# Optimization experiments

Hardware: AMD Instinct MI355X
Metric: run time of the kernel (lower is better)

The kernel has to match this reference:

```python
import jax, jax.numpy as jnp
import numpy as np

NUM_HEADS = 16
D_MODEL = 1024
DEPTH = D_MODEL // NUM_HEADS


def rope_sincos(seq_len, depth):
    # standard RoPE: inv_freq over even dims, sin/cos tiled to full depth
    inv_freq = 1.0 / (10000.0 ** (jnp.arange(0, depth, 2, dtype=jnp.float32) / depth))
    ang = jnp.arange(seq_len, dtype=jnp.float32)[:, None] * inv_freq[None, :]  # [S, depth/2]
    sin = jnp.concatenate([jnp.sin(ang), jnp.sin(ang)], axis=-1)  # [S, depth]
    cos = jnp.concatenate([jnp.cos(ang), jnp.cos(ang)], axis=-1)
    return sin, cos


def apply_rope(x, sin, cos):
    # x: [B,H,S,depth]; rotate-half formulation
    half = x.shape[-1] // 2
    x1, x2 = x[..., :half], x[..., half:]
    rot = jnp.concatenate([-x2, x1], axis=-1)
    return x * cos + rot * sin


def setup_inputs() -> dict:
    key = jax.random.key(0)
    ks = jax.random.split(key, 5)
    s = 1.0 / np.sqrt(D_MODEL)
    return {
        "x": jax.random.normal(ks[0], (2, 2048, D_MODEL), dtype=jnp.float32),
        "wq": jax.random.normal(ks[1], (D_MODEL, D_MODEL), dtype=jnp.float32) * s,
        "bq": jnp.zeros((D_MODEL,), jnp.float32),
        "wk": jax.random.normal(ks[2], (D_MODEL, D_MODEL), dtype=jnp.float32) * s,
        "bk": jnp.zeros((D_MODEL,), jnp.float32),
        "wv": jax.random.normal(ks[3], (D_MODEL, D_MODEL), dtype=jnp.float32) * s,
        "bv": jnp.zeros((D_MODEL,), jnp.float32),
        "wo": jax.random.normal(ks[4], (D_MODEL, D_MODEL), dtype=jnp.float32) * s,
        "bo": jnp.zeros((D_MODEL,), jnp.float32),
    }


def reference(x, wq, bq, wk, bk, wv, bv, wo, bo):
    B, S, _ = x.shape

    def split_heads(t):  # [B,S,D] -> [B,H,S,depth]
        return t.reshape(B, S, NUM_HEADS, DEPTH).transpose(0, 2, 1, 3)

    Q = split_heads(x @ wq + bq)
    K = split_heads(x @ wk + bk)
    V = split_heads(x @ wv + bv)

    sin, cos = rope_sincos(S, DEPTH)  # [S, depth], broadcasts over B,H
    Q = apply_rope(Q, sin, cos)
    K = apply_rope(K, sin, cos)

    scores = jnp.einsum("bhqd,bhkd->bhqk", Q, K) / jnp.sqrt(jnp.float32(DEPTH))
    weights = jax.nn.softmax(scores, axis=-1)
    out = jnp.einsum("bhqk,bhkd->bhqd", weights, V)
    out = out.transpose(0, 2, 1, 3).reshape(B, S, D_MODEL)
    return out @ wo + bo
```

## Files before the change

kernel.cpp:

```cpp
#include <hip/hip_runtime.h>

#define DM 1024
#define SEQ 2048
#define NH 16
#define DH 64
#define BATCH 2

typedef _Float16 half_t;
typedef _Float16 half8 __attribute__((ext_vector_type(8)));
typedef _Float16 half4 __attribute__((ext_vector_type(4)));
typedef float f32x4 __attribute__((ext_vector_type(4)));

__device__ __forceinline__ f32x4 mfma16(half8 a, half8 b, f32x4 c) {
  return __builtin_amdgcn_mfma_f32_16x16x32_f16(a, b, c, 0, 0, 0);
}

__device__ __forceinline__ void gl2lds16(const half_t* g, half_t* l) {
  __builtin_amdgcn_global_load_lds((const __attribute__((address_space(1))) void*)g,
                                   (__attribute__((address_space(3))) void*)l, 16, 0, 0);
}


__global__ void cvt_x_kernel(const float* __restrict__ x, half_t* __restrict__ xh) {
  int i = (blockIdx.x * 256 + threadIdx.x) * 4;
  float4 v = *(const float4*)(x + i);
  half4 h = { (half_t)v.x, (half_t)v.y, (half_t)v.z, (half_t)v.w };
  *(half4*)(xh + i) = h;
}

__global__ void wtrans_kernel(const float* __restrict__ w0, const float* __restrict__ w1,
                              const float* __restrict__ w2, const float* __restrict__ w3,
                              half_t* __restrict__ o0, half_t* __restrict__ o1,
                              half_t* __restrict__ o2, half_t* __restrict__ o3) {
  __shared__ float tile[32][33];
  const float* w = (blockIdx.z == 0) ? w0 : (blockIdx.z == 1) ? w1 : (blockIdx.z == 2) ? w2 : w3;
  half_t* o = (blockIdx.z == 0) ? o0 : (blockIdx.z == 1) ? o1 : (blockIdx.z == 2) ? o2 : o3;
  int tx = threadIdx.x, ty0 = threadIdx.y;
  int bx = blockIdx.x * 32, by = blockIdx.y * 32;
#pragma unroll
  for (int i = 0; i < 4; i++) {
    int ty = ty0 + i * 8;
    tile[ty][tx] = w[(size_t)(by + ty) * DM + bx + tx];
  }
  __syncthreads();
#pragma unroll
  for (int i = 0; i < 4; i++) {
    int ty = ty0 + i * 8;
    o[(size_t)(bx + ty) * DM + by + tx] = (half_t)tile[tx][ty];
  }
}

__global__ void ropetab_kernel(float* __restrict__ st, float* __restrict__ ct) {
  int idx = blockIdx.x * 256 + threadIdx.x;
  int s = idx >> 5, i = idx & 31;
  float freq = exp2f(-(float)i * (13.287712379549449f / 32.0f));
  float ang = (float)s * freq;
  st[idx] = sinf(ang);
  ct[idx] = cosf(ang);
}

__global__ __launch_bounds__(256)
void vtrans_kernel(const half_t* __restrict__ Vh, half_t* __restrict__ Vt) {
  __shared__ half_t t[64 * 72];
  const int tid = threadIdx.x;
  const int bh = blockIdx.y;
  const int s0 = blockIdx.x * 64;
  const half_t* src = Vh + (size_t)bh * SEQ * DH + (size_t)s0 * DH;
  half_t* dst = Vt + (size_t)bh * DH * SEQ;
#pragma unroll
  for (int i = 0; i < 2; i++) {
    int s = tid + i * 256;
    int row = s >> 3, blk = s & 7;
    *(half8*)&t[row * 72 + blk * 8] = *(const half8*)&src[(size_t)row * DH + blk * 8];
  }
  __syncthreads();
  const int d = tid >> 2;
#pragma unroll
  for (int i = 0; i < 2; i++) {
    int sb = (tid & 3) * 8 + i * 32;
    half8 v;
#pragma unroll
    for (int j = 0; j < 8; j++) v[j] = t[(sb + j) * 72 + d];
    *(half8*)&dst[(size_t)d * SEQ + s0 + sb] = v;
  }
}


__global__ __launch_bounds__(256)
void qkv_kernel(const half_t* __restrict__ xh,
                const half_t* __restrict__ wtq, const half_t* __restrict__ wtk,
                const half_t* __restrict__ wtv,
                const float* __restrict__ bq, const float* __restrict__ bk,
                const float* __restrict__ bv,
                const float* __restrict__ st, const float* __restrict__ ctab,
                half_t* __restrict__ Qh, half_t* __restrict__ Kh, half_t* __restrict__ Vh) {
  const int tid = threadIdx.x;
  const int wid = tid >> 6, lane = tid & 63;
  const int l16 = lane & 15, quad = lane >> 4;
  const int g = blockIdx.z;
  const int m0 = blockIdx.y * 128, n0 = blockIdx.x * 128;
  const half_t* wt = (g == 0) ? wtq : (g == 1) ? wtk : wtv;
  const float* bias = (g == 0) ? bq : (g == 1) ? bk : bv;
  __shared__ __align__(16) half_t As[128 * 64];
  __shared__ __align__(16) half_t Bs[128 * 64];
  f32x4 acc[4][4] = {};
  const int wrow = (wid >> 1) * 64, wcol = (wid & 1) * 64;

  const int r0 = tid >> 3,         b0 = (tid & 7) ^ (r0 & 7);
  const int r1 = (tid + 256) >> 3, b1 = (tid & 7) ^ (r1 & 7);
  const int r2 = (tid + 512) >> 3, b2 = (tid & 7) ^ (r2 & 7);
  const int r3 = (tid + 768) >> 3, b3 = (tid & 7) ^ (r3 & 7);
  const int pb0 = (quad ^ (l16 & 7)) * 8;
  const int pb1 = ((4 + quad) ^ (l16 & 7)) * 8;

  for (int k0 = 0; k0 < DM; k0 += 64) {
    __syncthreads();
    gl2lds16(&xh[(size_t)(m0 + r0) * DM + k0 + b0 * 8], &As[tid * 8]);
    gl2lds16(&xh[(size_t)(m0 + r1) * DM + k0 + b1 * 8], &As[(tid + 256) * 8]);
    gl2lds16(&xh[(size_t)(m0 + r2) * DM + k0 + b2 * 8], &As[(tid + 512) * 8]);
    gl2lds16(&xh[(size_t)(m0 + r3) * DM + k0 + b3 * 8], &As[(tid + 768) * 8]);
    gl2lds16(&wt[(size_t)(n0 + r0) * DM + k0 + b0 * 8], &Bs[tid * 8]);
    gl2lds16(&wt[(size_t)(n0 + r1) * DM + k0 + b1 * 8], &Bs[(tid + 256) * 8]);
    gl2lds16(&wt[(size_t)(n0 + r2) * DM + k0 + b2 * 8], &Bs[(tid + 512) * 8]);
    gl2lds16(&wt[(size_t)(n0 + r3) * DM + k0 + b3 * 8], &Bs[(tid + 768) * 8]);
    __syncthreads();
    half8 a[2][4], b[2][4];
#pragma unroll
    for (int rt = 0; rt < 4; rt++) {
      a[0][rt] = *(const half8*)&As[(wrow + rt * 16 + l16) * 64 + pb0];
      a[1][rt] = *(const half8*)&As[(wrow + rt * 16 + l16) * 64 + pb1];
    }
#pragma unroll
    for (int ct = 0; ct < 4; ct++) {
      b[0][ct] = *(const half8*)&Bs[(wcol + ct * 16 + l16) * 64 + pb0];
      b[1][ct] = *(const half8*)&Bs[(wcol + ct * 16 + l16) * 64 + pb1];
    }
#pragma unroll
    for (int kk = 0; kk < 2; kk++)
#pragma unroll
      for (int rt = 0; rt < 4; rt++)
#pragma unroll
        for (int ct = 0; ct < 4; ct++)
          acc[rt][ct] = mfma16(a[kk][rt], b[kk][ct], acc[rt][ct]);
  }

  const int h = (n0 + wcol) >> 6;
  const float qscale = 0.125f * 1.44269504089f;
  half_t* dst = (g == 0) ? Qh : (g == 1) ? Kh : Vh;
  float bv4[4];
#pragma unroll
  for (int ct = 0; ct < 4; ct++) bv4[ct] = bias[n0 + wcol + ct * 16 + l16];
#pragma unroll
  for (int rt = 0; rt < 4; rt++) {
#pragma unroll
    for (int r = 0; r < 4; r++) {
      int m = m0 + wrow + rt * 16 + quad * 4 + r;
      int bb = m >> 11, s = m & 2047;
      float v0 = acc[rt][0][r] + bv4[0];
      float v1 = acc[rt][1][r] + bv4[1];
      float v2 = acc[rt][2][r] + bv4[2];
      float v3 = acc[rt][3][r] + bv4[3];
      float o0 = v0, o1 = v1, o2 = v2, o3 = v3;
      if (g != 2) {
        float sn0 = st[s * 32 + l16], cs0 = ctab[s * 32 + l16];
        float sn1 = st[s * 32 + 16 + l16], cs1 = ctab[s * 32 + 16 + l16];
        o0 = v0 * cs0 - v2 * sn0;
        o1 = v1 * cs1 - v3 * sn1;
        o2 = v2 * cs0 + v0 * sn0;
        o3 = v3 * cs1 + v1 * sn1;
        if (g == 0) { o0 *= qscale; o1 *= qscale; o2 *= qscale; o3 *= qscale; }
      }
      size_t base = ((size_t)(bb * NH + h) * SEQ + s) * DH;
      dst[base + l16]      = (half_t)o0;
      dst[base + 16 + l16] = (half_t)o1;
      dst[base + 32 + l16] = (half_t)o2;
      dst[base + 48 + l16] = (half_t)o3;
    }
  }
}


__global__ __launch_bounds__(256)
void attn_kernel(const half_t* __restrict__ Qh, const half_t* __restrict__ Kh,
                 const half_t* __restrict__ Vt, half_t* __restrict__ AO) {
  const int tid = threadIdx.x;
  const int wid = tid >> 6, lane = tid & 63;
  const int l16 = lane & 15, quad = lane >> 4;
  const int bh = blockIdx.x;
  const int bb = bh >> 4, h = bh & 15;
  const int q0 = blockIdx.y * 128 + wid * 32;
  const half_t* Q = Qh + (size_t)bh * SEQ * DH;
  const half_t* K = Kh + (size_t)bh * SEQ * DH;
  const half_t* V = Vt + (size_t)bh * DH * SEQ;
  __shared__ __align__(16) half_t Ks[64 * 64];
  __shared__ __align__(16) half_t Vs[64 * 64];
  __shared__ __align__(16) half_t pbuf[4][32 * 72];
  half_t* myp = pbuf[wid];

  const int r0 = tid >> 3,         c0 = (tid & 7) ^ (r0 & 7);
  const int r1 = (tid + 256) >> 3, c1 = (tid & 7) ^ (r1 & 7);
  const int sw0 = ((quad ^ (l16 & 7)) * 8);
  const int sw1 = (((quad + 4) ^ (l16 & 7)) * 8);

  half8 aqA0 = *(const half8*)&Q[(size_t)(q0 + l16) * DH + quad * 8];
  half8 aqA1 = *(const half8*)&Q[(size_t)(q0 + l16) * DH + 32 + quad * 8];
  half8 aqB0 = *(const half8*)&Q[(size_t)(q0 + 16 + l16) * DH + quad * 8];
  half8 aqB1 = *(const half8*)&Q[(size_t)(q0 + 16 + l16) * DH + 32 + quad * 8];
  f32x4 oA[4] = {}, oB[4] = {};
  float lrowA[4] = {0.f, 0.f, 0.f, 0.f}, lrowB[4] = {0.f, 0.f, 0.f, 0.f};
  const f32x4 cinit = {-12.f, -12.f, -12.f, -12.f};

  for (int kb0 = 0; kb0 < SEQ; kb0 += 64) {
    __syncthreads();
    gl2lds16(&K[(size_t)(kb0 + r0) * DH + c0 * 8], &Ks[tid * 8]);
    gl2lds16(&K[(size_t)(kb0 + r1) * DH + c1 * 8], &Ks[(tid + 256) * 8]);
    gl2lds16(&V[(size_t)r0 * SEQ + kb0 + c0 * 8], &Vs[tid * 8]);
    gl2lds16(&V[(size_t)r1 * SEQ + kb0 + c1 * 8], &Vs[(tid + 256) * 8]);
    __syncthreads();

    f32x4 sfA[4], sfB[4];
#pragma unroll
    for (int kt = 0; kt < 4; kt++) {
      const half_t* krow = &Ks[(kt * 16 + l16) * 64];
      half8 b0 = *(const half8*)&krow[sw0];
      half8 b1 = *(const half8*)&krow[sw1];
      f32x4 zA = cinit, zB = cinit;
      zA = mfma16(aqA0, b0, zA);
      zA = mfma16(aqA1, b1, zA);
      zB = mfma16(aqB0, b0, zB);
      zB = mfma16(aqB1, b1, zB);
      sfA[kt] = zA; sfB[kt] = zB;
    }
#pragma unroll
    for (int kt = 0; kt < 4; kt++)
#pragma unroll
      for (int r = 0; r < 4; r++) {
        float pA = __builtin_amdgcn_exp2f(sfA[kt][r]);
        float pB = __builtin_amdgcn_exp2f(sfB[kt][r]);
        lrowA[r] += pA;
        lrowB[r] += pB;
        myp[(quad * 4 + r) * 72 + kt * 16 + l16] = (half_t)pA;
        myp[(16 + quad * 4 + r) * 72 + kt * 16 + l16] = (half_t)pB;
      }
    half8 apA0 = *(const half8*)&myp[l16 * 72 + quad * 8];
    half8 apA1 = *(const half8*)&myp[l16 * 72 + 32 + quad * 8];
    half8 apB0 = *(const half8*)&myp[(16 + l16) * 72 + quad * 8];
    half8 apB1 = *(const half8*)&myp[(16 + l16) * 72 + 32 + quad * 8];
#pragma unroll
    for (int dt = 0; dt < 4; dt++) {
      const half_t* vrow = &Vs[(dt * 16 + l16) * 64];
      half8 bv0 = *(const half8*)&vrow[sw0];
      half8 bv1 = *(const half8*)&vrow[sw1];
      oA[dt] = mfma16(apA0, bv0, oA[dt]);
      oA[dt] = mfma16(apA1, bv1, oA[dt]);
      oB[dt] = mfma16(apB0, bv0, oB[dt]);
      oB[dt] = mfma16(apB1, bv1, oB[dt]);
    }
  }
#pragma unroll
  for (int d = 1; d <= 8; d <<= 1)
#pragma unroll
    for (int r = 0; r < 4; r++) {
      lrowA[r] += __shfl_xor(lrowA[r], d);
      lrowB[r] += __shfl_xor(lrowB[r], d);
    }
#pragma unroll
  for (int r = 0; r < 4; r++) { lrowA[r] = 1.f / lrowA[r]; lrowB[r] = 1.f / lrowB[r]; }
#pragma unroll
  for (int dt = 0; dt < 4; dt++)
#pragma unroll
    for (int r = 0; r < 4; r++) {
      int srowA = q0 + quad * 4 + r;
      int srowB = q0 + 16 + quad * 4 + r;
      AO[((size_t)bb * SEQ + srowA) * DM + h * DH + dt * 16 + l16] = (half_t)(oA[dt][r] * lrowA[r]);
      AO[((size_t)bb * SEQ + srowB) * DM + h * DH + dt * 16 + l16] = (half_t)(oB[dt][r] * lrowB[r]);
    }
}


__global__ __launch_bounds__(256)
void out_kernel(const half_t* __restrict__ AO, const half_t* __restrict__ wto,
                const float* __restrict__ bo, float* __restrict__ out) {
  const int tid = threadIdx.x;
  const int wid = tid >> 6, lane = tid & 63;
  const int l16 = lane & 15, quad = lane >> 4;
  const int m0 = blockIdx.y * 128, n0 = blockIdx.x * 64;
  __shared__ __align__(16) half_t As[128 * 64];
  __shared__ __align__(16) half_t Bs[64 * 64];
  f32x4 acc[4][2] = {};
  const int wrow = (wid >> 1) * 64, wcol = (wid & 1) * 32;

  const int r0 = tid >> 3,         b0 = (tid & 7) ^ (r0 & 7);
  const int r1 = (tid + 256) >> 3, b1 = (tid & 7) ^ (r1 & 7);
  const int r2 = (tid + 512) >> 3, b2 = (tid & 7) ^ (r2 & 7);
  const int r3 = (tid + 768) >> 3, b3 = (tid & 7) ^ (r3 & 7);
  const int pb0 = (quad ^ (l16 & 7)) * 8;
  const int pb1 = ((4 + quad) ^ (l16 & 7)) * 8;

  for (int k0 = 0; k0 < DM; k0 += 64) {
    __syncthreads();
    gl2lds16(&AO[(size_t)(m0 + r0) * DM + k0 + b0 * 8], &As[tid * 8]);
    gl2lds16(&AO[(size_t)(m0 + r1) * DM + k0 + b1 * 8], &As[(tid + 256) * 8]);
    gl2lds16(&AO[(size_t)(m0 + r2) * DM + k0 + b2 * 8], &As[(tid + 512) * 8]);
    gl2lds16(&AO[(size_t)(m0 + r3) * DM + k0 + b3 * 8], &As[(tid + 768) * 8]);
    gl2lds16(&wto[(size_t)(n0 + r0) * DM + k0 + b0 * 8], &Bs[tid * 8]);
    gl2lds16(&wto[(size_t)(n0 + r1) * DM + k0 + b1 * 8], &Bs[(tid + 256) * 8]);
    __syncthreads();
    half8 a[2][4], b[2][2];
#pragma unroll
    for (int rt = 0; rt < 4; rt++) {
      a[0][rt] = *(const half8*)&As[(wrow + rt * 16 + l16) * 64 + pb0];
      a[1][rt] = *(const half8*)&As[(wrow + rt * 16 + l16) * 64 + pb1];
    }
#pragma unroll
    for (int ct = 0; ct < 2; ct++) {
      b[0][ct] = *(const half8*)&Bs[(wcol + ct * 16 + l16) * 64 + pb0];
      b[1][ct] = *(const half8*)&Bs[(wcol + ct * 16 + l16) * 64 + pb1];
    }
#pragma unroll
    for (int kk = 0; kk < 2; kk++)
#pragma unroll
      for (int rt = 0; rt < 4; rt++)
#pragma unroll
        for (int ct = 0; ct < 2; ct++)
          acc[rt][ct] = mfma16(a[kk][rt], b[kk][ct], acc[rt][ct]);
  }
  float bv2[2];
#pragma unroll
  for (int ct = 0; ct < 2; ct++) bv2[ct] = bo[n0 + wcol + ct * 16 + l16];
#pragma unroll
  for (int rt = 0; rt < 4; rt++)
#pragma unroll
    for (int r = 0; r < 4; r++) {
      int m = m0 + wrow + rt * 16 + quad * 4 + r;
#pragma unroll
      for (int ct = 0; ct < 2; ct++)
        out[(size_t)m * DM + n0 + wcol + ct * 16 + l16] = acc[rt][ct][r] + bv2[ct];
    }
}


extern "C" void kernel_launch(void* const* d_in, const int* in_sizes, int n_in,
                              void* d_out, int out_size, void* d_ws, size_t ws_size,
                              hipStream_t stream) {
  (void)in_sizes; (void)n_in; (void)out_size; (void)ws_size;
  const float* x  = (const float*)d_in[0];
  const float* wq = (const float*)d_in[1];
  const float* bq = (const float*)d_in[2];
  const float* wk = (const float*)d_in[3];
  const float* bk = (const float*)d_in[4];
  const float* wv = (const float*)d_in[5];
  const float* bv = (const float*)d_in[6];
  const float* wo = (const float*)d_in[7];
  const float* bo = (const float*)d_in[8];
  char* ws = (char*)d_ws;
  const size_t MB = 1u << 20;
  half_t* xh  = (half_t*)(ws + 0);
  half_t* AO  = (half_t*)(ws + 0);
  half_t* wtq = (half_t*)(ws + 8 * MB);
  half_t* wtk = (half_t*)(ws + 10 * MB);
  half_t* wtv = (half_t*)(ws + 12 * MB);
  half_t* wto = (half_t*)(ws + 14 * MB);
  float*  st  = (float*)(ws + 16 * MB);
  float*  ctb = (float*)(ws + 16 * MB + 256 * 1024);
  half_t* Qh  = (half_t*)(ws + 17 * MB);
  half_t* Kh  = (half_t*)(ws + 25 * MB);
  half_t* Vh  = (half_t*)(ws + 33 * MB);
  half_t* Vt  = (half_t*)(ws + 41 * MB);
  float* out = (float*)d_out;

  cvt_x_kernel<<<4096, 256, 0, stream>>>(x, xh);
  wtrans_kernel<<<dim3(32, 32, 4), dim3(32, 8), 0, stream>>>(wq, wk, wv, wo, wtq, wtk, wtv, wto);
  ropetab_kernel<<<256, 256, 0, stream>>>(st, ctb);
  qkv_kernel<<<dim3(8, 32, 3), 256, 0, stream>>>(xh, wtq, wtk, wtv, bq, bk, bv, st, ctb, Qh, Kh, Vh);
  vtrans_kernel<<<dim3(32, 32), 256, 0, stream>>>(Vh, Vt);
  attn_kernel<<<dim3(32, 16), 256, 0, stream>>>(Qh, Kh, Vt, AO);
  out_kernel<<<dim3(16, 32), 256, 0, stream>>>(AO, wto, bo, out);
}
```

Before: 218.6 us.

## Double-buffer LDS tiles in QKV, attention and output kernels

```diff
diff --git a/kernel.cpp b/kernel.cpp
--- a/kernel.cpp
+++ b/kernel.cpp
@@ -101,47 +101,42 @@
   const int m0 = blockIdx.y * 128, n0 = blockIdx.x * 128;
   const half_t* wt = (g == 0) ? wtq : (g == 1) ? wtk : wtv;
   const float* bias = (g == 0) ? bq : (g == 1) ? bk : bv;
-  __shared__ __align__(16) half_t As[128 * 64];
-  __shared__ __align__(16) half_t Bs[128 * 64];
+  __shared__ __align__(16) half_t As[2][128 * 32];
+  __shared__ __align__(16) half_t Bs[2][128 * 32];
   f32x4 acc[4][4] = {};
   const int wrow = (wid >> 1) * 64, wcol = (wid & 1) * 64;
 
-  const int r0 = tid >> 3,         b0 = (tid & 7) ^ (r0 & 7);
-  const int r1 = (tid + 256) >> 3, b1 = (tid & 7) ^ (r1 & 7);
-  const int r2 = (tid + 512) >> 3, b2 = (tid & 7) ^ (r2 & 7);
-  const int r3 = (tid + 768) >> 3, b3 = (tid & 7) ^ (r3 & 7);
-  const int pb0 = (quad ^ (l16 & 7)) * 8;
-  const int pb1 = ((4 + quad) ^ (l16 & 7)) * 8;
-
-  for (int k0 = 0; k0 < DM; k0 += 64) {
+  const int ar0 = tid >> 2,          ab0 = (tid & 3) ^ ((ar0 >> 1) & 3);
+  const int ar1 = (tid + 256) >> 2,  ab1 = (tid & 3) ^ ((ar1 >> 1) & 3);
+  const int swz = (l16 >> 1) & 3;
+
+  gl2lds16(&xh[(size_t)(m0 + ar0) * DM + ab0 * 8], &As[0][tid * 8]);
+  gl2lds16(&xh[(size_t)(m0 + ar1) * DM + ab1 * 8], &As[0][(tid + 256) * 8]);
+  gl2lds16(&wt[(size_t)(n0 + ar0) * DM + ab0 * 8], &Bs[0][tid * 8]);
+  gl2lds16(&wt[(size_t)(n0 + ar1) * DM + ab1 * 8], &Bs[0][(tid + 256) * 8]);
+
+  int cur = 0;
+  for (int k0 = 0; k0 < DM; k0 += 32, cur ^= 1) {
     __syncthreads();
-    gl2lds16(&xh[(size_t)(m0 + r0) * DM + k0 + b0 * 8], &As[tid * 8]);
-    gl2lds16(&xh[(size_t)(m0 + r1) * DM + k0 + b1 * 8], &As[(tid + 256) * 8]);
-    gl2lds16(&xh[(size_t)(m0 + r2) * DM + k0 + b2 * 8], &As[(tid + 512) * 8]);
-    gl2lds16(&xh[(size_t)(m0 + r3) * DM + k0 + b3 * 8], &As[(tid + 768) * 8]);
-    gl2lds16(&wt[(size_t)(n0 + r0) * DM + k0 + b0 * 8], &Bs[tid * 8]);
-    gl2lds16(&wt[(size_t)(n0 + r1) * DM + k0 + b1 * 8], &Bs[(tid + 256) * 8]);
-    gl2lds16(&wt[(size_t)(n0 + r2) * DM + k0 + b2 * 8], &Bs[(tid + 512) * 8]);
-    gl2lds16(&wt[(size_t)(n0 + r3) * DM + k0 + b3 * 8], &Bs[(tid + 768) * 8]);
-    __syncthreads();
-    half8 a[2][4], b[2][4];
-#pragma unroll
-    for (int rt = 0; rt < 4; rt++) {
-      a[0][rt] = *(const half8*)&As[(wrow + rt * 16 + l16) * 64 + pb0];
-      a[1][rt] = *(const half8*)&As[(wrow + rt * 16 + l16) * 64 + pb1];
-    }
-#pragma unroll
-    for (int ct = 0; ct < 4; ct++) {
-      b[0][ct] = *(const half8*)&Bs[(wcol + ct * 16 + l16) * 64 + pb0];
-      b[1][ct] = *(const half8*)&Bs[(wcol + ct * 16 + l16) * 64 + pb1];
-    }
-#pragma unroll
-    for (int kk = 0; kk < 2; kk++)
-#pragma unroll
-      for (int rt = 0; rt < 4; rt++)
-#pragma unroll
-        for (int ct = 0; ct < 4; ct++)
-          acc[rt][ct] = mfma16(a[kk][rt], b[kk][ct], acc[rt][ct]);
+    int kn = k0 + 32;
+    if (kn < DM) {
+      gl2lds16(&xh[(size_t)(m0 + ar0) * DM + kn + ab0 * 8], &As[cur ^ 1][tid * 8]);
+      gl2lds16(&xh[(size_t)(m0 + ar1) * DM + kn + ab1 * 8], &As[cur ^ 1][(tid + 256) * 8]);
+      gl2lds16(&wt[(size_t)(n0 + ar0) * DM + kn + ab0 * 8], &Bs[cur ^ 1][tid * 8]);
+      gl2lds16(&wt[(size_t)(n0 + ar1) * DM + kn + ab1 * 8], &Bs[cur ^ 1][(tid + 256) * 8]);
+    }
+    half8 a[4], b[4];
+#pragma unroll
+    for (int rt = 0; rt < 4; rt++)
+      a[rt] = *(const half8*)&As[cur][((wrow + rt * 16 + l16) * 4 + (quad ^ swz)) * 8];
+#pragma unroll
+    for (int ct = 0; ct < 4; ct++)
+      b[ct] = *(const half8*)&Bs[cur][((wcol + ct * 16 + l16) * 4 + (quad ^ swz)) * 8];
+#pragma unroll
+    for (int rt = 0; rt < 4; rt++)
+#pragma unroll
+      for (int ct = 0; ct < 4; ct++)
+        acc[rt][ct] = mfma16(a[rt], b[ct], acc[rt][ct]);
   }
 
   const int h = (n0 + wcol) >> 6;
@@ -192,8 +187,8 @@
   const half_t* Q = Qh + (size_t)bh * SEQ * DH;
   const half_t* K = Kh + (size_t)bh * SEQ * DH;
   const half_t* V = Vt + (size_t)bh * DH * SEQ;
-  __shared__ __align__(16) half_t Ks[64 * 64];
-  __shared__ __align__(16) half_t Vs[64 * 64];
+  __shared__ __align__(16) half_t Ks[2][64 * 64];
+  __shared__ __align__(16) half_t Vs[2][64 * 64];
   __shared__ __align__(16) half_t pbuf[4][32 * 72];
   half_t* myp = pbuf[wid];
 
@@ -210,18 +205,26 @@
   float lrowA[4] = {0.f, 0.f, 0.f, 0.f}, lrowB[4] = {0.f, 0.f, 0.f, 0.f};
   const f32x4 cinit = {-12.f, -12.f, -12.f, -12.f};
 
-  for (int kb0 = 0; kb0 < SEQ; kb0 += 64) {
+  gl2lds16(&K[(size_t)r0 * DH + c0 * 8], &Ks[0][tid * 8]);
+  gl2lds16(&K[(size_t)r1 * DH + c1 * 8], &Ks[0][(tid + 256) * 8]);
+  gl2lds16(&V[(size_t)r0 * SEQ + c0 * 8], &Vs[0][tid * 8]);
+  gl2lds16(&V[(size_t)r1 * SEQ + c1 * 8], &Vs[0][(tid + 256) * 8]);
+
+  int cur = 0;
+  for (int kb0 = 0; kb0 < SEQ; kb0 += 64, cur ^= 1) {
     __syncthreads();
-    gl2lds16(&K[(size_t)(kb0 + r0) * DH + c0 * 8], &Ks[tid * 8]);
-    gl2lds16(&K[(size_t)(kb0 + r1) * DH + c1 * 8], &Ks[(tid + 256) * 8]);
-    gl2lds16(&V[(size_t)r0 * SEQ + kb0 + c0 * 8], &Vs[tid * 8]);
-    gl2lds16(&V[(size_t)r1 * SEQ + kb0 + c1 * 8], &Vs[(tid + 256) * 8]);
-    __syncthreads();
+    int kn = kb0 + 64;
+    if (kn < SEQ) {
+      gl2lds16(&K[(size_t)(kn + r0) * DH + c0 * 8], &Ks[cur ^ 1][tid * 8]);
+      gl2lds16(&K[(size_t)(kn + r1) * DH + c1 * 8], &Ks[cur ^ 1][(tid + 256) * 8]);
+      gl2lds16(&V[(size_t)r0 * SEQ + kn + c0 * 8], &Vs[cur ^ 1][tid * 8]);
+      gl2lds16(&V[(size_t)r1 * SEQ + kn + c1 * 8], &Vs[cur ^ 1][(tid + 256) * 8]);
+    }
 
     f32x4 sfA[4], sfB[4];
 #pragma unroll
     for (int kt = 0; kt < 4; kt++) {
-      const half_t* krow = &Ks[(kt * 16 + l16) * 64];
+      const half_t* krow = &Ks[cur][(kt * 16 + l16) * 64];
       half8 b0 = *(const half8*)&krow[sw0];
       half8 b1 = *(const half8*)&krow[sw1];
       f32x4 zA = cinit, zB = cinit;
@@ -248,7 +251,7 @@
     half8 apB1 = *(const half8*)&myp[(16 + l16) * 72 + 32 + quad * 8];
 #pragma unroll
     for (int dt = 0; dt < 4; dt++) {
-      const half_t* vrow = &Vs[(dt * 16 + l16) * 64];
+      const half_t* vrow = &Vs[cur][(dt * 16 + l16) * 64];
       half8 bv0 = *(const half8*)&vrow[sw0];
       half8 bv1 = *(const half8*)&vrow[sw1];
       oA[dt] = mfma16(apA0, bv0, oA[dt]);
@@ -285,45 +288,40 @@
   const int wid = tid >> 6, lane = tid & 63;
   const int l16 = lane & 15, quad = lane >> 4;
   const int m0 = blockIdx.y * 128, n0 = blockIdx.x * 64;
-  __shared__ __align__(16) half_t As[128 * 64];
-  __shared__ __align__(16) half_t Bs[64 * 64];
+  __shared__ __align__(16) half_t As[2][128 * 32];
+  __shared__ __align__(16) half_t Bs[2][64 * 32];
   f32x4 acc[4][2] = {};
   const int wrow = (wid >> 1) * 64, wcol = (wid & 1) * 32;
 
-  const int r0 = tid >> 3,         b0 = (tid & 7) ^ (r0 & 7);
-  const int r1 = (tid + 256) >> 3, b1 = (tid & 7) ^ (r1 & 7);
-  const int r2 = (tid + 512) >> 3, b2 = (tid & 7) ^ (r2 & 7);
-  const int r3 = (tid + 768) >> 3, b3 = (tid & 7) ^ (r3 & 7);
-  const int pb0 = (quad ^ (l16 & 7)) * 8;
-  const int pb1 = ((4 + quad) ^ (l16 & 7)) * 8;
-
-  for (int k0 = 0; k0 < DM; k0 += 64) {
+  const int ar0 = tid >> 2,         ab0 = (tid & 3) ^ ((ar0 >> 1) & 3);
+  const int ar1 = (tid + 256) >> 2, ab1 = (tid & 3) ^ ((ar1 >> 1) & 3);
+  const int swz = (l16 >> 1) & 3;
+
+  gl2lds16(&AO[(size_t)(m0 + ar0) * DM + ab0 * 8], &As[0][tid * 8]);
+  gl2lds16(&AO[(size_t)(m0 + ar1) * DM + ab1 * 8], &As[0][(tid + 256) * 8]);
+  gl2lds16(&wto[(size_t)(n0 + ar0) * DM + ab0 * 8], &Bs[0][tid * 8]);
+
+  int cur = 0;
+  for (int k0 = 0; k0 < DM; k0 += 32, cur ^= 1) {
     __syncthreads();
-    gl2lds16(&AO[(size_t)(m0 + r0) * DM + k0 + b0 * 8], &As[tid * 8]);
-    gl2lds16(&AO[(size_t)(m0 + r1) * DM + k0 + b1 * 8], &As[(tid + 256) * 8]);
-    gl2lds16(&AO[(size_t)(m0 + r2) * DM + k0 + b2 * 8], &As[(tid + 512) * 8]);
-    gl2lds16(&AO[(size_t)(m0 + r3) * DM + k0 + b3 * 8], &As[(tid + 768) * 8]);
-    gl2lds16(&wto[(size_t)(n0 + r0) * DM + k0 + b0 * 8], &Bs[tid * 8]);
-    gl2lds16(&wto[(size_t)(n0 + r1) * DM + k0 + b1 * 8], &Bs[(tid + 256) * 8]);
-    __syncthreads();
-    half8 a[2][4], b[2][2];
-#pragma unroll
-    for (int rt = 0; rt < 4; rt++) {
-      a[0][rt] = *(const half8*)&As[(wrow + rt * 16 + l16) * 64 + pb0];
-      a[1][rt] = *(const half8*)&As[(wrow + rt * 16 + l16) * 64 + pb1];
-    }
-#pragma unroll
-    for (int ct = 0; ct < 2; ct++) {
-      b[0][ct] = *(const half8*)&Bs[(wcol + ct * 16 + l16) * 64 + pb0];
-      b[1][ct] = *(const half8*)&Bs[(wcol + ct * 16 + l16) * 64 + pb1];
-    }
-#pragma unroll
-    for (int kk = 0; kk < 2; kk++)
-#pragma unroll
-      for (int rt = 0; rt < 4; rt++)
-#pragma unroll
-        for (int ct = 0; ct < 2; ct++)
-          acc[rt][ct] = mfma16(a[kk][rt], b[kk][ct], acc[rt][ct]);
+    int kn = k0 + 32;
+    if (kn < DM) {
+      gl2lds16(&AO[(size_t)(m0 + ar0) * DM + kn + ab0 * 8], &As[cur ^ 1][tid * 8]);
+      gl2lds16(&AO[(size_t)(m0 + ar1) * DM + kn + ab1 * 8], &As[cur ^ 1][(tid + 256) * 8]);
+      gl2lds16(&wto[(size_t)(n0 + ar0) * DM + kn + ab0 * 8], &Bs[cur ^ 1][tid * 8]);
+    }
+    half8 a[4], b[2];
+#pragma unroll
+    for (int rt = 0; rt < 4; rt++)
+      a[rt] = *(const half8*)&As[cur][((wrow + rt * 16 + l16) * 4 + (quad ^ swz)) * 8];
+#pragma unroll
+    for (int ct = 0; ct < 2; ct++)
+      b[ct] = *(const half8*)&Bs[cur][((wcol + ct * 16 + l16) * 4 + (quad ^ swz)) * 8];
+#pragma unroll
+    for (int rt = 0; rt < 4; rt++)
+#pragma unroll
+      for (int ct = 0; ct < 2; ct++)
+        acc[rt][ct] = mfma16(a[rt], b[ct], acc[rt][ct]);
   }
   float bv2[2];
 #pragma unroll
```

Result: faster. 212.9 us (-2.6%).
